# Kernel optimization log

Hardware: AMD Instinct MI355X
Metric: run time of the kernel (lower is better)

The kernel has to match this reference:

```python
import jax, jax.numpy as jnp
import numpy as np

B, T, C = 2, 2048, 1024
H = 16
D = C // H
SCALE = 0.1 / (D ** 0.5)  # nonstandard 0.1/sqrt(head_dim) scale from source


def setup_inputs() -> dict:
    key = jax.random.key(0)
    ks = jax.random.split(key, 5)
    s = 0.02
    return {
        "x": jax.random.normal(ks[0], (B, T, C), jnp.float32),
        "w_attn": jax.random.normal(ks[1], (C, 3 * C), jnp.float32) * s,
        "b_attn": jax.random.normal(ks[2], (3 * C,), jnp.float32) * s,
        "w_proj": jax.random.normal(ks[3], (C, C), jnp.float32) * s,
        "b_proj": jax.random.normal(ks[4], (C,), jnp.float32) * s,
    }


def reference(x, w_attn, b_attn, w_proj, b_proj):
    Bs, Ts, Cs = x.shape
    qkv = x @ w_attn + b_attn                      # [B,T,3C]
    q, k, v = jnp.split(qkv, 3, axis=-1)
    q = q.reshape(Bs, Ts, H, D)                    # [B,T,H,D]
    k = k.reshape(Bs, Ts, H, D)
    v = v.reshape(Bs, Ts, H, D)
    attn = jnp.einsum("bthd,bshd->bhts", q, k) * SCALE  # [B,H,T,T]
    causal = jnp.tril(jnp.ones((Ts, Ts), dtype=bool))
    attn = jnp.where(causal, attn, -jnp.inf)
    attn = jax.nn.softmax(attn, axis=-1)
    y = jnp.einsum("bhts,bshd->bthd", attn, v).reshape(Bs, Ts, Cs)
    return y @ w_proj + b_proj
```

## Files before the change

### kernel.cpp

```cpp
#include <hip/hip_runtime.h>


#define Bz 2
#define Tz 2048
#define Cz 1024
#define Hz 16
#define Dz 64
#define QSCALE 0.01803368801111437f
#define KSS 76
#define VTS 74

typedef unsigned short u16;
typedef short bf16x4 __attribute__((ext_vector_type(4)));
typedef short bf16x8 __attribute__((ext_vector_type(8)));
typedef float f32x4 __attribute__((ext_vector_type(4)));

#define MFMA32(A, B, C) __builtin_amdgcn_mfma_f32_16x16x32_bf16(A, B, C, 0, 0, 0)

__device__ inline f32x4 mfma16(bf16x4 a, bf16x4 b, f32x4 c) {
#if defined(__HIP_DEVICE_COMPILE__)
  return __builtin_amdgcn_mfma_f32_16x16x16bf16_1k(a, b, c, 0, 0, 0);
#else
  return c;
#endif
}

__device__ inline u16 f2bf(float f) {
  return (u16)((__float_as_uint(f) + 0x8000u) >> 16);
}

__device__ inline float fexp2(float x) {
#if __has_builtin(__builtin_amdgcn_exp2f)
  return __builtin_amdgcn_exp2f(x);
#else
  return exp2f(x);
#endif
}

__device__ inline void gl_lds16(const u16* g, u16* l) {
  __builtin_amdgcn_global_load_lds(
      (const __attribute__((address_space(1))) void*)g,
      (__attribute__((address_space(3))) void*)l, 16, 0, 0);
}

#define NCAST 4096
#define NTA   3072
__global__ __launch_bounds__(256) void prep_kernel(const float* __restrict__ x,
                                                   const float* __restrict__ wa,
                                                   const float* __restrict__ wp,
                                                   u16* __restrict__ xb,
                                                   u16* __restrict__ waT,
                                                   u16* __restrict__ wpT) {
  const int bx = blockIdx.x, t = threadIdx.x;
  if (bx < NCAST) {
    int i = bx * 256 + t;
    float4 v = ((const float4*)x)[i];
    ushort4 o = {f2bf(v.x), f2bf(v.y), f2bf(v.z), f2bf(v.w)};
    ((ushort4*)xb)[i] = o;
    return;
  }
  __shared__ float tile[32][33];
  const float* W;
  u16* WT;
  int N, idx;
  if (bx < NCAST + NTA) {
    W = wa; WT = waT; N = 3 * Cz; idx = bx - NCAST;
  } else {
    W = wp; WT = wpT; N = Cz; idx = bx - NCAST - NTA;
  }
  const int n0 = (idx % (N / 32)) * 32, k0 = (idx / (N / 32)) * 32;
  const int tx = t & 31, ty = t >> 5;
#pragma unroll
  for (int i = 0; i < 4; ++i)
    tile[ty + 8 * i][tx] = W[(size_t)(k0 + ty + 8 * i) * N + n0 + tx];
  __syncthreads();
#pragma unroll
  for (int i = 0; i < 4; ++i)
    WT[(size_t)(n0 + ty + 8 * i) * Cz + k0 + tx] = f2bf(tile[tx][ty + 8 * i]);
}

template <bool OUT_BF16, int TN>
__global__ __launch_bounds__(256) void gemm_bt(const u16* __restrict__ A,
                                               const u16* __restrict__ BT,
                                               const float* __restrict__ bias,
                                               void* __restrict__ Cout,
                                               int M, int N, int K,
                                               int qcols, float qscale) {
  __shared__ __align__(16) u16 As[128 * 64];
  __shared__ __align__(16) u16 Bs[TN * 64];
  constexpr int NT = TN / 32;
  const int t = threadIdx.x;
  const int wave = t >> 6, lane = t & 63;
  const int lm = lane & 15, lg = lane >> 4;
  const int wm = wave >> 1, wn = wave & 1;
  const int m0 = blockIdx.y * 128, n0 = blockIdx.x * TN;

  const int lrow = lane >> 3;
  const int gseg = (lane & 7) ^ lrow;
  const size_t a_base = (size_t)(m0 + 32 * wave + lrow) * K + gseg * 8;
  u16* const a_lds = &As[(32 * wave) * 64];
  const size_t b_base = (size_t)(n0 + (TN / 4) * wave + lrow) * K + gseg * 8;
  u16* const b_lds = &Bs[((TN / 4) * wave) * 64];

  f32x4 acc[4][NT];
#pragma unroll
  for (int mt = 0; mt < 4; ++mt)
#pragma unroll
    for (int nt = 0; nt < NT; ++nt)
#pragma unroll
      for (int i = 0; i < 4; ++i) acc[mt][nt][i] = 0.f;

  for (int k0 = 0; k0 < K; k0 += 64) {
    __syncthreads();
#pragma unroll
    for (int i = 0; i < 4; ++i)
      gl_lds16(A + a_base + (size_t)(8 * i) * K + k0, a_lds + i * 8 * 64);
#pragma unroll
    for (int i = 0; i < NT; ++i)
      gl_lds16(BT + b_base + (size_t)(8 * i) * K + k0, b_lds + i * 8 * 64);
    __syncthreads();

#pragma unroll
    for (int h = 0; h < 2; ++h) {
      const int rs = ((lg + 4 * h) ^ (lm & 7)) * 8;
      bf16x8 af[4], bfr[NT];
#pragma unroll
      for (int mt = 0; mt < 4; ++mt)
        af[mt] = *(const bf16x8*)&As[(64 * wm + 16 * mt + lm) * 64 + rs];
#pragma unroll
      for (int nt = 0; nt < NT; ++nt)
        bfr[nt] = *(const bf16x8*)&Bs[((TN / 2) * wn + 16 * nt + lm) * 64 + rs];
#pragma unroll
      for (int mt = 0; mt < 4; ++mt)
#pragma unroll
        for (int nt = 0; nt < NT; ++nt)
          acc[mt][nt] = MFMA32(af[mt], bfr[nt], acc[mt][nt]);
    }
  }

#pragma unroll
  for (int nt = 0; nt < NT; ++nt) {
    int gc = n0 + (TN / 2) * wn + 16 * nt + lm;
    float bv = bias[gc];
    float sc = (gc < qcols) ? qscale : 1.f;
#pragma unroll
    for (int mt = 0; mt < 4; ++mt) {
#pragma unroll
      for (int i = 0; i < 4; ++i) {
        int gr = m0 + 64 * wm + 16 * mt + 4 * lg + i;
        float v = (acc[mt][nt][i] + bv) * sc;
        if (OUT_BF16)
          ((u16*)Cout)[(size_t)gr * N + gc] = f2bf(v);
        else
          ((float*)Cout)[(size_t)gr * N + gc] = v;
      }
    }
  }
}

__global__ __launch_bounds__(256) void attn_kernel(const u16* __restrict__ qkv,
                                                   u16* __restrict__ yb) {
  __shared__ __align__(16) u16 Ks[2][64][KSS];
  __shared__ __align__(16) u16 Vt[2][64][VTS];

  const int t = threadIdx.x;
  const int wave = t >> 6, lane = t & 63;
  const int lm = lane & 15, lg = lane >> 4;
  const int kg8 = lg << 3;
  const int x = blockIdx.x;
  const int bh = x & 31, qtp = x >> 5;
  const int qt = (qtp < 16) ? qtp : 47 - qtp;
  const int b = bh >> 4, h = bh & 15;
  const int q0 = qt * 64;
  const size_t rowstride = 3 * Cz;
  const u16* qbase = qkv + (size_t)b * Tz * rowstride + h * Dz;

  bf16x8 qf[2];
  {
    const u16* qrow = qbase + (size_t)(q0 + wave * 16 + lm) * rowstride + kg8;
    qf[0] = *(const bf16x8*)qrow;
    qf[1] = *(const bf16x8*)(qrow + 32);
  }

  float psum = 0.f;
  f32x4 Oa[4];
#pragma unroll
  for (int i = 0; i < 4; ++i)
#pragma unroll
    for (int j = 0; j < 4; ++j) Oa[i][j] = 0.f;

  const int ksr = t >> 2, kds = (t & 3) << 4;
  const int vsp = t & 31, vds = (t >> 5) << 3;
  const u16* kbase = qbase + Cz + (size_t)ksr * rowstride + kds;
  const u16* vbase = qbase + 2 * Cz + (size_t)(2 * vsp) * rowstride + vds;
  const size_t tilestep = 64 * rowstride;

  uint4 kr[2], vr[2];
  auto load_tile = [&](int kt) {
    const u16* kp = kbase + (size_t)kt * tilestep;
    const u16* vp = vbase + (size_t)kt * tilestep;
    kr[0] = *(const uint4*)kp;
    kr[1] = *(const uint4*)(kp + 8);
    vr[0] = *(const uint4*)vp;
    vr[1] = *(const uint4*)(vp + rowstride);
  };
  auto stage_write = [&](int buf) {
    *(uint4*)&Ks[buf][ksr][kds] = kr[0];
    *(uint4*)&Ks[buf][ksr][kds + 8] = kr[1];
    unsigned av[4] = {vr[0].x, vr[0].y, vr[0].z, vr[0].w};
    unsigned cv[4] = {vr[1].x, vr[1].y, vr[1].z, vr[1].w};
#pragma unroll
    for (int j = 0; j < 4; ++j) {
      unsigned w0 = (av[j] & 0xffffu) | (cv[j] << 16);
      unsigned w1 = (av[j] >> 16) | (cv[j] & 0xffff0000u);
      *(unsigned*)&Vt[buf][vds + 2 * j][2 * vsp] = w0;
      *(unsigned*)&Vt[buf][vds + 2 * j + 1][2 * vsp] = w1;
    }
  };

  load_tile(0);
  stage_write(0);
  load_tile(1);

  for (int kt = 0; kt <= qt; ++kt) {
    __syncthreads();
    const int cb = kt & 1;
    if (kt + 1 <= qt) {
      stage_write(1 - cb);
      if (kt + 2 <= qt) load_tile(kt + 2);
    }

    f32x4 S[4];
#pragma unroll
    for (int c = 0; c < 4; ++c) {
      bf16x8 k0 = *(const bf16x8*)&Ks[cb][c * 16 + lm][kg8];
      bf16x8 k1 = *(const bf16x8*)&Ks[cb][c * 16 + lm][32 + kg8];
      f32x4 s;
#pragma unroll
      for (int i = 0; i < 4; ++i) s[i] = 0.f;
      s = MFMA32(k0, qf[0], s);
      s = MFMA32(k1, qf[1], s);
      S[c] = s;
    }

    const bool diag = (kt == qt);
    const int qloc = 16 * wave + lm;
    bf16x4 pf[4];
#pragma unroll
    for (int c = 0; c < 4; ++c) {
#pragma unroll
      for (int r = 0; r < 4; ++r) {
        float p = fexp2(S[c][r]);
        if (diag && (c * 16 + 4 * lg + r) > qloc) p = 0.f;
        psum += p;
        pf[c][r] = (short)f2bf(p);
      }
    }

#pragma unroll
    for (int dt = 0; dt < 4; ++dt) {
#pragma unroll
      for (int c = 0; c < 4; ++c) {
        bf16x4 vfr = *(const bf16x4*)&Vt[cb][16 * dt + lm][c * 16 + 4 * lg];
        Oa[dt] = mfma16(pf[c], vfr, Oa[dt]);
      }
    }
  }

  float s = psum;
  s += __shfl_xor(s, 16);
  s += __shfl_xor(s, 32);
  const float linv = 1.f / s;
  float invq[4];
#pragma unroll
  for (int r = 0; r < 4; ++r)
    invq[r] = __shfl(linv, 20 * lg + r);
  __syncthreads();
#pragma unroll
  for (int dt = 0; dt < 4; ++dt)
#pragma unroll
    for (int r = 0; r < 4; ++r)
      Ks[0][16 * wave + 4 * lg + r][16 * dt + lm] = f2bf(Oa[dt][r] * invq[r]);
  __syncthreads();
  {
    const int row = lane >> 2, seg = lane & 3;
    const uint4* src = (const uint4*)&Ks[0][16 * wave + row][seg * 16];
    uint4 v0 = src[0];
    uint4 v1 = src[1];
    u16* dst = yb + (size_t)(b * Tz + q0 + 16 * wave + row) * Cz + h * Dz + seg * 16;
    *(uint4*)dst = v0;
    *(uint4*)(dst + 8) = v1;
  }
}

extern "C" void kernel_launch(void* const* d_in, const int* in_sizes, int n_in,
                              void* d_out, int out_size, void* d_ws, size_t ws_size,
                              hipStream_t stream) {
  const float* x      = (const float*)d_in[0];
  const float* w_attn = (const float*)d_in[1];
  const float* b_attn = (const float*)d_in[2];
  const float* w_proj = (const float*)d_in[3];
  const float* b_proj = (const float*)d_in[4];

  char* ws = (char*)d_ws;
  u16* xb   = (u16*)(ws);
  u16* waT  = (u16*)(ws + (8ull << 20));
  u16* wpT  = (u16*)(ws + (14ull << 20));
  u16* qkvb = (u16*)(ws + (16ull << 20));
  u16* yb   = (u16*)(ws + (40ull << 20));

  const int M = Bz * Tz;

  prep_kernel<<<NCAST + NTA + 1024, 256, 0, stream>>>(x, w_attn, w_proj, xb, waT, wpT);
  gemm_bt<true, 128><<<dim3(3 * Cz / 128, M / 128), 256, 0, stream>>>(
      xb, waT, b_attn, qkvb, M, 3 * Cz, Cz, Cz, QSCALE);
  attn_kernel<<<1024, 256, 0, stream>>>(qkvb, yb);
  gemm_bt<false, 64><<<dim3(Cz / 64, M / 128), 256, 0, stream>>>(
      yb, wpT, b_proj, d_out, M, Cz, Cz, 0, 1.f);
}
```

Baseline: 203.6 us.

## Emit transposed V from QKV GEMM and stage K/V via direct global-to-LDS loads

The QKV GEMM epilogue now writes the V columns into a separate per-(batch, feature) transposed buffer, so attention no longer transposes V in registers before writing it to shared memory. The attention kernel replaces its register-staged K/V loads with asynchronous global-to-LDS copies (gl_lds16) into XOR-swizzled 64x64 tiles, with matching swizzled fragment reads. This removes register staging and the permute work from the inner loop and lets the copies overlap compute. The cost is extra strided epilogue stores in the GEMM and an added workspace buffer.

```diff
diff --git a/kernel.cpp b/kernel.cpp
--- a/kernel.cpp
+++ b/kernel.cpp
@@ -7,8 +7,6 @@
 #define Hz 16
 #define Dz 64
 #define QSCALE 0.01803368801111437f
-#define KSS 76
-#define VTS 74
 
 typedef unsigned short u16;
 typedef short bf16x4 __attribute__((ext_vector_type(4)));
@@ -79,11 +77,12 @@
     WT[(size_t)(n0 + ty + 8 * i) * Cz + k0 + tx] = f2bf(tile[tx][ty + 8 * i]);
 }
 
-template <bool OUT_BF16, int TN>
+template <bool OUT_BF16, int TN, bool VSPLIT>
 __global__ __launch_bounds__(256) void gemm_bt(const u16* __restrict__ A,
                                                const u16* __restrict__ BT,
                                                const float* __restrict__ bias,
                                                void* __restrict__ Cout,
+                                               u16* __restrict__ vTout,
                                                int M, int N, int K,
                                                int qcols, float qscale) {
   __shared__ __align__(16) u16 As[128 * 64];
@@ -142,6 +141,18 @@
   for (int nt = 0; nt < NT; ++nt) {
     int gc = n0 + (TN / 2) * wn + 16 * nt + lm;
     float bv = bias[gc];
+    if (VSPLIT && gc >= 2 * Cz) {
+      const int dg = gc - 2 * Cz;
+#pragma unroll
+      for (int mt = 0; mt < 4; ++mt) {
+        const int gr0 = m0 + 64 * wm + 16 * mt + 4 * lg;
+        const int bb = gr0 >> 11, s0 = gr0 & 2047;
+        ushort4 o = {f2bf(acc[mt][nt][0] + bv), f2bf(acc[mt][nt][1] + bv),
+                     f2bf(acc[mt][nt][2] + bv), f2bf(acc[mt][nt][3] + bv)};
+        *(ushort4*)(vTout + (((size_t)(bb * 1024 + dg)) << 11) + s0) = o;
+      }
+      continue;
+    }
     float sc = (gc < qcols) ? qscale : 1.f;
 #pragma unroll
     for (int mt = 0; mt < 4; ++mt) {
@@ -159,14 +170,14 @@
 }
 
 __global__ __launch_bounds__(256) void attn_kernel(const u16* __restrict__ qkv,
+                                                   const u16* __restrict__ vT,
                                                    u16* __restrict__ yb) {
-  __shared__ __align__(16) u16 Ks[2][64][KSS];
-  __shared__ __align__(16) u16 Vt[2][64][VTS];
+  __shared__ __align__(16) u16 KsL[2][64 * 64];
+  __shared__ __align__(16) u16 VtL[2][64 * 64];
 
   const int t = threadIdx.x;
   const int wave = t >> 6, lane = t & 63;
   const int lm = lane & 15, lg = lane >> 4;
-  const int kg8 = lg << 3;
   const int x = blockIdx.x;
   const int bh = x & 31, qtp = x >> 5;
   const int qt = (qtp < 16) ? qtp : 47 - qtp;
@@ -174,10 +185,11 @@
   const int q0 = qt * 64;
   const size_t rowstride = 3 * Cz;
   const u16* qbase = qkv + (size_t)b * Tz * rowstride + h * Dz;
+  const u16* vTbh = vT + ((size_t)(b * Hz + h) * Dz) * Tz;
 
   bf16x8 qf[2];
   {
-    const u16* qrow = qbase + (size_t)(q0 + wave * 16 + lm) * rowstride + kg8;
+    const u16* qrow = qbase + (size_t)(q0 + wave * 16 + lm) * rowstride + (lg << 3);
     qf[0] = *(const bf16x8*)qrow;
     qf[1] = *(const bf16x8*)(qrow + 32);
   }
@@ -189,52 +201,34 @@
 #pragma unroll
     for (int j = 0; j < 4; ++j) Oa[i][j] = 0.f;
 
-  const int ksr = t >> 2, kds = (t & 3) << 4;
-  const int vsp = t & 31, vds = (t >> 5) << 3;
-  const u16* kbase = qbase + Cz + (size_t)ksr * rowstride + kds;
-  const u16* vbase = qbase + 2 * Cz + (size_t)(2 * vsp) * rowstride + vds;
-  const size_t tilestep = 64 * rowstride;
-
-  uint4 kr[2], vr[2];
-  auto load_tile = [&](int kt) {
-    const u16* kp = kbase + (size_t)kt * tilestep;
-    const u16* vp = vbase + (size_t)kt * tilestep;
-    kr[0] = *(const uint4*)kp;
-    kr[1] = *(const uint4*)(kp + 8);
-    vr[0] = *(const uint4*)vp;
-    vr[1] = *(const uint4*)(vp + rowstride);
+  const int srow = lane >> 3;
+  const int sgl = ((lane & 7) ^ srow) * 8;
+  const u16* kstg = qbase + Cz + (size_t)(16 * wave + srow) * rowstride + sgl;
+  const u16* vstg = vTbh + (size_t)(16 * wave + srow) * Tz + sgl;
+
+  auto stage_issue = [&](int kt, int buf) {
+#pragma unroll
+    for (int c2 = 0; c2 < 2; ++c2) {
+      gl_lds16(kstg + (size_t)(8 * c2) * rowstride + (size_t)(64 * kt) * rowstride,
+               &KsL[buf][(16 * wave + 8 * c2) * 64]);
+      gl_lds16(vstg + (size_t)(8 * c2) * Tz + 64 * kt,
+               &VtL[buf][(16 * wave + 8 * c2) * 64]);
+    }
   };
-  auto stage_write = [&](int buf) {
-    *(uint4*)&Ks[buf][ksr][kds] = kr[0];
-    *(uint4*)&Ks[buf][ksr][kds + 8] = kr[1];
-    unsigned av[4] = {vr[0].x, vr[0].y, vr[0].z, vr[0].w};
-    unsigned cv[4] = {vr[1].x, vr[1].y, vr[1].z, vr[1].w};
-#pragma unroll
-    for (int j = 0; j < 4; ++j) {
-      unsigned w0 = (av[j] & 0xffffu) | (cv[j] << 16);
-      unsigned w1 = (av[j] >> 16) | (cv[j] & 0xffff0000u);
-      *(unsigned*)&Vt[buf][vds + 2 * j][2 * vsp] = w0;
-      *(unsigned*)&Vt[buf][vds + 2 * j + 1][2 * vsp] = w1;
-    }
-  };
-
-  load_tile(0);
-  stage_write(0);
-  load_tile(1);
+
+  stage_issue(0, 0);
 
   for (int kt = 0; kt <= qt; ++kt) {
     __syncthreads();
     const int cb = kt & 1;
-    if (kt + 1 <= qt) {
-      stage_write(1 - cb);
-      if (kt + 2 <= qt) load_tile(kt + 2);
-    }
+    if (kt + 1 <= qt) stage_issue(kt + 1, 1 - cb);
 
     f32x4 S[4];
 #pragma unroll
     for (int c = 0; c < 4; ++c) {
-      bf16x8 k0 = *(const bf16x8*)&Ks[cb][c * 16 + lm][kg8];
-      bf16x8 k1 = *(const bf16x8*)&Ks[cb][c * 16 + lm][32 + kg8];
+      const int rb = (16 * c + lm) * 64;
+      bf16x8 k0 = *(const bf16x8*)&KsL[cb][rb + ((lg ^ (lm & 7)) << 3)];
+      bf16x8 k1 = *(const bf16x8*)&KsL[cb][rb + (((lg + 4) ^ (lm & 7)) << 3)];
       f32x4 s;
 #pragma unroll
       for (int i = 0; i < 4; ++i) s[i] = 0.f;
@@ -259,9 +253,11 @@
 
 #pragma unroll
     for (int dt = 0; dt < 4; ++dt) {
+      const int rb = (16 * dt + lm) * 64;
 #pragma unroll
       for (int c = 0; c < 4; ++c) {
-        bf16x4 vfr = *(const bf16x4*)&Vt[cb][16 * dt + lm][c * 16 + 4 * lg];
+        const int off = (((2 * c + (lg >> 1)) ^ (lm & 7)) << 3) + 4 * (lg & 1);
+        bf16x4 vfr = *(const bf16x4*)&VtL[cb][rb + off];
         Oa[dt] = mfma16(pf[c], vfr, Oa[dt]);
       }
     }
@@ -280,11 +276,12 @@
   for (int dt = 0; dt < 4; ++dt)
 #pragma unroll
     for (int r = 0; r < 4; ++r)
-      Ks[0][16 * wave + 4 * lg + r][16 * dt + lm] = f2bf(Oa[dt][r] * invq[r]);
+      KsL[0][(16 * wave + 4 * lg + r) * 64 + 16 * dt + lm] =
+          f2bf(Oa[dt][r] * invq[r]);
   __syncthreads();
   {
     const int row = lane >> 2, seg = lane & 3;
-    const uint4* src = (const uint4*)&Ks[0][16 * wave + row][seg * 16];
+    const uint4* src = (const uint4*)&KsL[0][(16 * wave + row) * 64 + seg * 16];
     uint4 v0 = src[0];
     uint4 v1 = src[1];
     u16* dst = yb + (size_t)(b * Tz + q0 + 16 * wave + row) * Cz + h * Dz + seg * 16;
@@ -308,13 +305,14 @@
   u16* wpT  = (u16*)(ws + (14ull << 20));
   u16* qkvb = (u16*)(ws + (16ull << 20));
   u16* yb   = (u16*)(ws + (40ull << 20));
+  u16* vTt  = (u16*)(ws + (48ull << 20));
 
   const int M = Bz * Tz;
 
   prep_kernel<<<NCAST + NTA + 1024, 256, 0, stream>>>(x, w_attn, w_proj, xb, waT, wpT);
-  gemm_bt<true, 128><<<dim3(3 * Cz / 128, M / 128), 256, 0, stream>>>(
-      xb, waT, b_attn, qkvb, M, 3 * Cz, Cz, Cz, QSCALE);
-  attn_kernel<<<1024, 256, 0, stream>>>(qkvb, yb);
-  gemm_bt<false, 64><<<dim3(Cz / 64, M / 128), 256, 0, stream>>>(
-      yb, wpT, b_proj, d_out, M, Cz, Cz, 0, 1.f);
-}
+  gemm_bt<true, 128, true><<<dim3(3 * Cz / 128, M / 128), 256, 0, stream>>>(
+      xb, waT, b_attn, qkvb, vTt, M, 3 * Cz, Cz, Cz, QSCALE);
+  attn_kernel<<<1024, 256, 0, stream>>>(qkvb, vTt, yb);
+  gemm_bt<false, 64, false><<<dim3(Cz / 64, M / 128), 256, 0, stream>>>(
+      yb, wpT, b_proj, d_out, nullptr, M, Cz, Cz, 0, 1.f);
+}
```

Result: faster. 171.4 us (-15.8%).
